# Optimization experiments

Hardware: AMD Instinct MI355X
Metric: run time of the kernel (lower is better)

Reference implementation:

```python
import math
import jax, jax.numpy as jnp
import numpy as np

EPS = 1e-7  # K.epsilon()
ANCHORS = np.array([[10, 14], [23, 27], [37, 58], [81, 82], [135, 169], [344, 319]], np.float32)
ANCHOR_MASK = [[3, 4, 5], [0, 1, 2]]  # tiny-yolo, num_layers = 2
NUM_CLASSES = 80
IGNORE_THRESH = 0.5


def _decode(feats, anchors, input_shape):
    # feats: (B,H,W,3*(5+C)) -> raw_pred (B,H,W,3,5+C), pred_xy, pred_wh (normalized xywh)
    B, H, W, _ = feats.shape
    na = anchors.shape[0]
    feats = feats.reshape(B, H, W, na, 5 + NUM_CLASSES)
    gy, gx = jnp.meshgrid(jnp.arange(H, dtype=feats.dtype), jnp.arange(W, dtype=feats.dtype), indexing='ij')
    grid = jnp.stack([gx, gy], -1)[None, :, :, None, :]  # (1,H,W,1,2) in (x,y)
    box_xy = (jax.nn.sigmoid(feats[..., :2]) + grid) / jnp.array([W, H], feats.dtype)
    box_wh = jnp.exp(feats[..., 2:4]) * anchors[None, None, None, :, :] / input_shape[::-1]
    return feats, box_xy, box_wh


def _box_ciou(b_true, b_pred):
    # b_true: (B,T,4) xywh, b_pred: (B,H,W,A,4) xywh -> ciou, iou: (B,H,W,A,T)
    bt = b_true[:, None, None, None, :, :]   # (B,1,1,1,T,4)
    bp = b_pred[..., None, :]                # (B,H,W,A,1,4)
    t_xy, t_wh = bt[..., :2], bt[..., 2:4]
    p_xy, p_wh = bp[..., :2], bp[..., 2:4]
    t_min, t_max = t_xy - t_wh / 2.0, t_xy + t_wh / 2.0
    p_min, p_max = p_xy - p_wh / 2.0, p_xy + p_wh / 2.0
    i_wh = jnp.maximum(jnp.minimum(t_max, p_max) - jnp.maximum(t_min, p_min), 0.0)
    inter = i_wh[..., 0] * i_wh[..., 1]
    union = t_wh[..., 0] * t_wh[..., 1] + p_wh[..., 0] * p_wh[..., 1] - inter
    iou = inter / (union + EPS)
    center = jnp.sum(jnp.square(t_xy - p_xy), -1)
    e_wh = jnp.maximum(jnp.maximum(t_max, p_max) - jnp.minimum(t_min, p_min), 0.0)
    diag = jnp.sum(jnp.square(e_wh), -1)
    diou = iou - center / (diag + EPS)
    v = 4.0 * jnp.square(jnp.arctan2(t_wh[..., 0], t_wh[..., 1]) - jnp.arctan2(p_wh[..., 0], p_wh[..., 1])) / (math.pi * math.pi)
    alpha = jax.lax.stop_gradient(v / (1.0 - iou + v + EPS))
    return diou - alpha * v, iou


def _bce_logits(target, logits):
    # numerically stable sigmoid BCE with logits (matches K.binary_crossentropy from_logits=True)
    return jnp.maximum(logits, 0.0) - logits * target + jnp.log1p(jnp.exp(-jnp.abs(logits)))


def setup_inputs() -> dict:
    key = jax.random.key(0)
    ks = jax.random.split(key, 10)
    B, T = 64, 100
    output0 = jax.random.normal(ks[0], (B, 13, 13, 255), jnp.float32) * 0.5
    output1 = jax.random.normal(ks[1], (B, 26, 26, 255), jnp.float32) * 0.5
    xy = jax.random.uniform(ks[2], (B, T, 2), jnp.float32)
    wh = jax.random.uniform(ks[3], (B, T, 2), jnp.float32, minval=0.05, maxval=0.3)
    y_true_box = jnp.concatenate([xy, wh], -1)
    iou_mask0 = (jax.random.uniform(ks[4], (B, 13, 13, 3, T)) < 0.01).astype(jnp.float32)
    iou_mask1 = (jax.random.uniform(ks[5], (B, 26, 26, 3, T)) < 0.01).astype(jnp.float32)
    class0 = jax.nn.one_hot(jax.random.randint(ks[6], (B, 13, 13, 3), 0, NUM_CLASSES), NUM_CLASSES) * (jax.random.uniform(ks[7], (B, 13, 13, 3, 1)) < 0.7)
    class1 = jax.nn.one_hot(jax.random.randint(ks[8], (B, 26, 26, 3), 0, NUM_CLASSES), NUM_CLASSES) * (jax.random.uniform(ks[9], (B, 26, 26, 3, 1)) < 0.7)
    return {"output0": output0, "output1": output1, "y_true_box": y_true_box,
            "iou_mask0": iou_mask0, "iou_mask1": iou_mask1, "class0": class0, "class1": class1}


def reference(output0, output1, y_true_box, iou_mask0, iou_mask1, class0, class1):
    outputs = [output0, output1]
    masks = [iou_mask0, iou_mask1]
    classes = [class0, class1]
    input_shape = jnp.asarray(output0.shape[1:3], jnp.float32) * 32.0  # (h,w)
    batch_f = jnp.float32(output0.shape[0])
    loss = total_loc = total_conf = total_cls = jnp.float32(0.0)
    for i in range(2):
        anchors = jnp.asarray(ANCHORS[ANCHOR_MASK[i]])
        raw_pred, pred_xy, pred_wh = _decode(outputs[i], anchors, input_shape)
        pred_box = jnp.concatenate([pred_xy, pred_wh], -1)  # (B,H,W,3,4)
        ciou, iou = _box_ciou(y_true_box, pred_box)         # (B,H,W,3,T)
        best_iou = jnp.max(iou, -1)                         # (B,H,W,3)
        ignore = (best_iou < IGNORE_THRESH)[..., None]
        ignore_match = (best_iou > IGNORE_THRESH)[..., None]
        class_id_match = jax.lax.stop_gradient(
            (jnp.max(jax.nn.sigmoid(raw_pred[..., 5:]), -1) < 0.25)[..., None] & ignore_match)
        ignore_mask = (ignore | class_id_match).astype(jnp.float32)
        ciou_loss = jnp.sum((1.0 - ciou) * masks[i], -1, keepdims=True)  # (B,H,W,3,1)
        obj = jnp.max(masks[i], -1, keepdims=True)  # true_objectness_probs
        bce_obj = _bce_logits(obj, raw_pred[..., 4:5])
        confidence_loss = obj * bce_obj + (1.0 - obj) * bce_obj * ignore_mask
        class_loss = obj * _bce_logits(classes[i], raw_pred[..., 5:])
        class_sum = jnp.sum(classes[i], -1, keepdims=True)
        class_sum = class_sum + (class_sum == 0).astype(jnp.float32)
        location_loss = jnp.sum(ciou_loss / class_sum) / batch_f
        confidence_loss = jnp.sum(confidence_loss) / batch_f
        class_loss = jnp.sum(class_loss) / batch_f
        loss = loss + location_loss + confidence_loss + class_loss
        total_loc = total_loc + location_loss
        total_conf = total_conf + confidence_loss
        total_cls = total_cls + class_loss
    return loss, total_loc, total_conf, total_cls
```

## Files before the change

### kernel.cpp

```cpp
#include <hip/hip_runtime.h>
#include <math.h>

#define T_BOX 100
#define NCLS 80
constexpr float EPSF = 1e-7f;
constexpr float INV416 = 1.0f / 416.0f;
constexpr float LOGIT25 = -1.0986122886681098f;

__device__ __forceinline__ float rcpf_(float x) { return __builtin_amdgcn_rcpf(x); }
__device__ __forceinline__ float sigmoidf_(float x) { return rcpf_(1.0f + __expf(-x)); }
__device__ __forceinline__ float softplus_abs_(float x) {
    return __logf(1.0f + __expf(-fabsf(x)));
}

__device__ __forceinline__ float atan2_pos_(float y, float x) {
    const float mn = fminf(y, x), mx = fmaxf(y, x);
    const float r  = mn * rcpf_(mx);
    const float r2 = r * r;
    float p = fmaf(r2, 0.0208351f, -0.0851330f);
    p = fmaf(r2, p, 0.1801410f);
    p = fmaf(r2, p, -0.3302995f);
    p = fmaf(r2, p, 0.9998660f);
    const float a = r * p;
    return (y > x) ? (1.5707963268f - a) : a;
}

__constant__ float c_anc[2][3][2] = {
    {{81.0f, 82.0f}, {135.0f, 169.0f}, {344.0f, 319.0f}},
    {{10.0f, 14.0f}, {23.0f, 27.0f}, {37.0f, 58.0f}},
};

#define CELLS0 507
#define CELLS1 2028
#define CELLS_TOT 2535
#define GRP_PER_BLK 16
#define NCHUNK 4
#define CELLS_PER_BLK 64
#define BLK_PER_BATCH 40

__device__ __forceinline__ float red16_add(float v) {
    v += __shfl_xor(v, 1); v += __shfl_xor(v, 2);
    v += __shfl_xor(v, 4); v += __shfl_xor(v, 8);
    return v;
}
__device__ __forceinline__ float red16_max(float v) {
    v = fmaxf(v, __shfl_xor(v, 1)); v = fmaxf(v, __shfl_xor(v, 2));
    v = fmaxf(v, __shfl_xor(v, 4)); v = fmaxf(v, __shfl_xor(v, 8));
    return v;
}

__global__ __launch_bounds__(256) void yolo_fused_kernel(
    const float* __restrict__ pred0, const float* __restrict__ mask0, const float* __restrict__ cls0,
    const float* __restrict__ pred1, const float* __restrict__ mask1, const float* __restrict__ cls1,
    const float* __restrict__ ytrue,
    float* __restrict__ ws, int nshard)
{
    __shared__ float4 s_box[T_BOX];
    __shared__ float4 s_aux[T_BOX];
    __shared__ float s_acc[6];

    const int b = blockIdx.y;
    const int tid = threadIdx.x;

    if (tid < T_BOX) {
        const float4 yt = *reinterpret_cast<const float4*>(ytrue + ((size_t)b * T_BOX + tid) * 4);
        s_box[tid] = make_float4(yt.x - 0.5f * yt.z, yt.y - 0.5f * yt.w,
                                 yt.x + 0.5f * yt.z, yt.y + 0.5f * yt.w);
        s_aux[tid] = make_float4(yt.x, yt.y, yt.z * yt.w, atan2_pos_(yt.z, yt.w));
    }
    if (tid < 6) s_acc[tid] = 0.0f;
    __syncthreads();

    const int l   = tid & 15;
    const int grp = tid >> 4;
    const float c4pi2 = 4.0f / (float)(M_PI * M_PI);

    #pragma unroll 1
    for (int chunk = 0; chunk < NCHUNK; ++chunk) {
        const int r = (int)blockIdx.x * CELLS_PER_BLK + chunk * GRP_PER_BLK + grp;
        if (r >= CELLS_TOT) break;

        int level, W, H, cell, ncell;
        const float *pred, *mask, *cls;
        float invWH;
        if (r < CELLS0) {
            level = 0; W = 13; H = 13; cell = r; ncell = CELLS0;
            invWH = 1.0f / 13.0f;
            pred = pred0; mask = mask0; cls = cls0;
        } else {
            level = 1; W = 26; H = 26; cell = r - CELLS0; ncell = CELLS1;
            invWH = 1.0f / 26.0f;
            pred = pred1; mask = mask1; cls = cls1;
        }

        const int a  = cell % 3;
        const int hw = cell / 3;
        const int w  = hw % W;
        const int h  = hw / W;

        const float* p = pred + ((size_t)((b * H + h) * W + w)) * 255 + a * 85;

        const float aw = c_anc[level][a][0];
        const float ah = c_anc[level][a][1];

        const float px = (sigmoidf_(p[0]) + (float)w) * invWH;
        const float py = (sigmoidf_(p[1]) + (float)h) * invWH;
        const float pw = __expf(p[2]) * aw * INV416;
        const float ph = __expf(p[3]) * ah * INV416;

        const float pminx = px - 0.5f * pw, pminy = py - 0.5f * ph;
        const float pmaxx = px + 0.5f * pw, pmaxy = py + 0.5f * ph;
        const float parea = pw * ph;
        const float patan = atan2_pos_(pw, ph);

        const float* m = mask + ((size_t)b * ncell + cell) * (size_t)T_BOX;

        float maxd = -1e30f, obj = 0.0f, locsum = 0.0f;

        float mv_[7];
        #pragma unroll
        for (int k = 0; k < 6; ++k) mv_[k] = m[l + 16 * k];
        mv_[6] = (l < 4) ? m[l + 96] : 0.0f;

        auto body = [&](int t, float mv) {
            const float4 bx = s_box[t];
            const float4 ax = s_aux[t];
            const float iwx = fmaxf(fminf(bx.z, pmaxx) - fmaxf(bx.x, pminx), 0.0f);
            const float iwy = fmaxf(fminf(bx.w, pmaxy) - fmaxf(bx.y, pminy), 0.0f);
            const float inter = iwx * iwy;
            const float sa = ax.z + parea;
            maxd = fmaxf(maxd, fmaf(3.0f, inter, -sa));
            obj  = fmaxf(obj, mv);
            if (mv != 0.0f) {
                const float uni = sa - inter;
                const float iou = inter * rcpf_(uni + EPSF);
                const float dx = ax.x - px, dy = ax.y - py;
                const float center = dx * dx + dy * dy;
                const float ewx = fmaxf(fmaxf(bx.z, pmaxx) - fminf(bx.x, pminx), 0.0f);
                const float ewy = fmaxf(fmaxf(bx.w, pmaxy) - fminf(bx.y, pminy), 0.0f);
                const float diag = ewx * ewx + ewy * ewy;
                const float diou = iou - center * rcpf_(diag + EPSF);
                const float dv = ax.w - patan;
                const float v = c4pi2 * dv * dv;
                const float alpha = v * rcpf_(1.0f - iou + v + EPSF);
                const float ciou = diou - alpha * v;
                locsum += (1.0f - ciou) * mv;
            }
        };

        #pragma unroll
        for (int k = 0; k < 6; ++k) body(l + 16 * k, mv_[k]);
        if (l < 4) body(l + 96, mv_[6]);

        obj  = red16_max(obj);
        maxd = red16_max(maxd);

        const float x4 = p[4];
        const float bce = fmaxf(x4, 0.0f) - x4 * obj + softplus_abs_(x4);

        float loc = 0.0f, conf, clsl = 0.0f;

        if (obj > 0.0f) {
            const float* cp = cls + ((size_t)b * ncell + cell) * (size_t)NCLS;
            float csum = 0.0f, bsum = 0.0f;
            #pragma unroll
            for (int k = 0; k < 5; ++k) {
                const int c = l + 16 * k;
                const float z = cp[c];
                const float x = p[5 + c];
                csum += z;
                bsum += fmaxf(x, 0.0f) - x * z + softplus_abs_(x);
            }
            locsum = red16_add(locsum);
            csum   = red16_add(csum);
            bsum   = red16_add(bsum);
            const float csum2 = csum + ((csum == 0.0f) ? 1.0f : 0.0f);
            loc  = locsum * rcpf_(csum2);
            clsl = bsum;
            conf = bce;
        } else {
            float ign;
            if (maxd > EPSF) {
                float maxlogit = -1e30f;
                #pragma unroll
                for (int k = 0; k < 5; ++k) maxlogit = fmaxf(maxlogit, p[5 + l + 16 * k]);
                maxlogit = red16_max(maxlogit);
                ign = (maxlogit < LOGIT25) ? 1.0f : 0.0f;
            } else {
                ign = (maxd < EPSF) ? 1.0f : 0.0f;
            }
            conf = bce * ign;
        }

        if (l == 0) {
            const int base = level * 3;
            atomicAdd(&s_acc[base + 0], loc);
            atomicAdd(&s_acc[base + 1], conf);
            atomicAdd(&s_acc[base + 2], clsl);
        }
    }

    __syncthreads();
    if (tid < 6) {
        const int shard = (int)((blockIdx.y * gridDim.x + blockIdx.x) % (unsigned)nshard);
        atomicAdd(&ws[shard * 16 + tid], s_acc[tid]);
    }
}

__global__ void yolo_finalize(const float* __restrict__ ws,
                              float* __restrict__ out, float invB, int nshard) {
    __shared__ float s_sum[6];
    const int t = threadIdx.x;
    if (t < 6) {
        float s = 0.0f;
        for (int i = 0; i < nshard; ++i) s += ws[i * 16 + t];
        s_sum[t] = s;
    }
    __syncthreads();
    if (t == 0) {
        const float loc  = (s_sum[0] + s_sum[3]) * invB;
        const float conf = (s_sum[1] + s_sum[4]) * invB;
        const float cls  = (s_sum[2] + s_sum[5]) * invB;
        out[0] = loc + conf + cls;
        out[1] = loc;
        out[2] = conf;
        out[3] = cls;
    }
}

extern "C" void kernel_launch(void* const* d_in, const int* in_sizes, int n_in,
                              void* d_out, int out_size, void* d_ws, size_t ws_size,
                              hipStream_t stream) {
    const float* out0  = (const float*)d_in[0];
    const float* out1  = (const float*)d_in[1];
    const float* ytrue = (const float*)d_in[2];
    const float* m0    = (const float*)d_in[3];
    const float* m1    = (const float*)d_in[4];
    const float* c0    = (const float*)d_in[5];
    const float* c1    = (const float*)d_in[6];
    float* out = (float*)d_out;
    float* ws  = (float*)d_ws;

    const int B = in_sizes[0] / (13 * 13 * 255);

    int nshard = (int)(ws_size / 64);
    if (nshard < 1)  nshard = 1;
    if (nshard > 64) nshard = 64;
    const size_t zero_bytes = (nshard == 1) ? 24 : (size_t)nshard * 64;

    hipMemsetAsync(ws, 0, zero_bytes, stream);

    dim3 grid(BLK_PER_BATCH, B);
    yolo_fused_kernel<<<grid, 256, 0, stream>>>(
        out0, m0, c0, out1, m1, c1, ytrue, ws, nshard);

    yolo_finalize<<<1, 64, 0, stream>>>(ws, out, 1.0f / (float)B, nshard);
}
```

Before: 54.01 us.

## Use 8 lanes per cell, one cell per group, and split aux shared arrays

Each cell is now processed by 8 lanes instead of 16, and the per-block chunk loop is removed, so every group handles one cell and the grid grows to 80 blocks per batch. Each lane walks 12-13 target boxes, which gives more independent mask loads in flight and shortens the shuffle reductions by one step. The mask loads are hoisted ahead of the prediction decode. The float4 aux shared array is split into four scalar arrays so that the common path reads only the area. In exchange, the per-block setup of the shared box tables is repeated across twice as many blocks, and each lane holds more registers.

```diff
diff --git a/kernel.cpp b/kernel.cpp
--- a/kernel.cpp
+++ b/kernel.cpp
@@ -33,19 +33,17 @@
 #define CELLS0 507
 #define CELLS1 2028
 #define CELLS_TOT 2535
-#define GRP_PER_BLK 16
-#define NCHUNK 4
-#define CELLS_PER_BLK 64
-#define BLK_PER_BATCH 40
-
-__device__ __forceinline__ float red16_add(float v) {
-    v += __shfl_xor(v, 1); v += __shfl_xor(v, 2);
-    v += __shfl_xor(v, 4); v += __shfl_xor(v, 8);
+#define LPC 8
+#define GRP_PER_BLK 32
+#define BLK_PER_BATCH 80
+
+__device__ __forceinline__ float red8_add(float v) {
+    v += __shfl_xor(v, 1); v += __shfl_xor(v, 2); v += __shfl_xor(v, 4);
     return v;
 }
-__device__ __forceinline__ float red16_max(float v) {
+__device__ __forceinline__ float red8_max(float v) {
     v = fmaxf(v, __shfl_xor(v, 1)); v = fmaxf(v, __shfl_xor(v, 2));
-    v = fmaxf(v, __shfl_xor(v, 4)); v = fmaxf(v, __shfl_xor(v, 8));
+    v = fmaxf(v, __shfl_xor(v, 4));
     return v;
 }
 
@@ -56,7 +54,7 @@
     float* __restrict__ ws, int nshard)
 {
     __shared__ float4 s_box[T_BOX];
-    __shared__ float4 s_aux[T_BOX];
+    __shared__ float s_ar[T_BOX], s_tx[T_BOX], s_ty[T_BOX], s_at[T_BOX];
     __shared__ float s_acc[6];
 
     const int b = blockIdx.y;
@@ -66,20 +64,18 @@
         const float4 yt = *reinterpret_cast<const float4*>(ytrue + ((size_t)b * T_BOX + tid) * 4);
         s_box[tid] = make_float4(yt.x - 0.5f * yt.z, yt.y - 0.5f * yt.w,
                                  yt.x + 0.5f * yt.z, yt.y + 0.5f * yt.w);
-        s_aux[tid] = make_float4(yt.x, yt.y, yt.z * yt.w, atan2_pos_(yt.z, yt.w));
+        s_ar[tid] = yt.z * yt.w;
+        s_tx[tid] = yt.x; s_ty[tid] = yt.y;
+        s_at[tid] = atan2_pos_(yt.z, yt.w);
     }
     if (tid < 6) s_acc[tid] = 0.0f;
     __syncthreads();
 
-    const int l   = tid & 15;
-    const int grp = tid >> 4;
-    const float c4pi2 = 4.0f / (float)(M_PI * M_PI);
-
-    #pragma unroll 1
-    for (int chunk = 0; chunk < NCHUNK; ++chunk) {
-        const int r = (int)blockIdx.x * CELLS_PER_BLK + chunk * GRP_PER_BLK + grp;
-        if (r >= CELLS_TOT) break;
-
+    const int l   = tid & (LPC - 1);
+    const int grp = tid >> 3;
+    const int r   = (int)blockIdx.x * GRP_PER_BLK + grp;
+
+    if (r < CELLS_TOT) {
         int level, W, H, cell, ncell;
         const float *pred, *mask, *cls;
         float invWH;
@@ -99,6 +95,12 @@
         const int h  = hw / W;
 
         const float* p = pred + ((size_t)((b * H + h) * W + w)) * 255 + a * 85;
+        const float* m = mask + ((size_t)b * ncell + cell) * (size_t)T_BOX;
+
+        float mv_[13];
+        #pragma unroll
+        for (int k = 0; k < 12; ++k) mv_[k] = m[l + LPC * k];
+        mv_[12] = (l < 4) ? m[96 + l] : 0.0f;
 
         const float aw = c_anc[level][a][0];
         const float ah = c_anc[level][a][1];
@@ -112,35 +114,28 @@
         const float pmaxx = px + 0.5f * pw, pmaxy = py + 0.5f * ph;
         const float parea = pw * ph;
         const float patan = atan2_pos_(pw, ph);
-
-        const float* m = mask + ((size_t)b * ncell + cell) * (size_t)T_BOX;
+        const float c4pi2 = 4.0f / (float)(M_PI * M_PI);
 
         float maxd = -1e30f, obj = 0.0f, locsum = 0.0f;
-
-        float mv_[7];
-        #pragma unroll
-        for (int k = 0; k < 6; ++k) mv_[k] = m[l + 16 * k];
-        mv_[6] = (l < 4) ? m[l + 96] : 0.0f;
 
         auto body = [&](int t, float mv) {
             const float4 bx = s_box[t];
-            const float4 ax = s_aux[t];
             const float iwx = fmaxf(fminf(bx.z, pmaxx) - fmaxf(bx.x, pminx), 0.0f);
             const float iwy = fmaxf(fminf(bx.w, pmaxy) - fmaxf(bx.y, pminy), 0.0f);
             const float inter = iwx * iwy;
-            const float sa = ax.z + parea;
+            const float sa = s_ar[t] + parea;
             maxd = fmaxf(maxd, fmaf(3.0f, inter, -sa));
             obj  = fmaxf(obj, mv);
             if (mv != 0.0f) {
                 const float uni = sa - inter;
                 const float iou = inter * rcpf_(uni + EPSF);
-                const float dx = ax.x - px, dy = ax.y - py;
+                const float dx = s_tx[t] - px, dy = s_ty[t] - py;
                 const float center = dx * dx + dy * dy;
                 const float ewx = fmaxf(fmaxf(bx.z, pmaxx) - fminf(bx.x, pminx), 0.0f);
                 const float ewy = fmaxf(fmaxf(bx.w, pmaxy) - fminf(bx.y, pminy), 0.0f);
                 const float diag = ewx * ewx + ewy * ewy;
                 const float diou = iou - center * rcpf_(diag + EPSF);
-                const float dv = ax.w - patan;
+                const float dv = s_at[t] - patan;
                 const float v = c4pi2 * dv * dv;
                 const float alpha = v * rcpf_(1.0f - iou + v + EPSF);
                 const float ciou = diou - alpha * v;
@@ -149,11 +144,11 @@
         };
 
         #pragma unroll
-        for (int k = 0; k < 6; ++k) body(l + 16 * k, mv_[k]);
-        if (l < 4) body(l + 96, mv_[6]);
-
-        obj  = red16_max(obj);
-        maxd = red16_max(maxd);
+        for (int k = 0; k < 12; ++k) body(l + LPC * k, mv_[k]);
+        if (l < 4) body(96 + l, mv_[12]);
+
+        obj  = red8_max(obj);
+        maxd = red8_max(maxd);
 
         const float x4 = p[4];
         const float bce = fmaxf(x4, 0.0f) - x4 * obj + softplus_abs_(x4);
@@ -164,16 +159,16 @@
             const float* cp = cls + ((size_t)b * ncell + cell) * (size_t)NCLS;
             float csum = 0.0f, bsum = 0.0f;
             #pragma unroll
-            for (int k = 0; k < 5; ++k) {
-                const int c = l + 16 * k;
+            for (int k = 0; k < 10; ++k) {
+                const int c = l + LPC * k;
                 const float z = cp[c];
                 const float x = p[5 + c];
                 csum += z;
                 bsum += fmaxf(x, 0.0f) - x * z + softplus_abs_(x);
             }
-            locsum = red16_add(locsum);
-            csum   = red16_add(csum);
-            bsum   = red16_add(bsum);
+            locsum = red8_add(locsum);
+            csum   = red8_add(csum);
+            bsum   = red8_add(bsum);
             const float csum2 = csum + ((csum == 0.0f) ? 1.0f : 0.0f);
             loc  = locsum * rcpf_(csum2);
             clsl = bsum;
@@ -183,8 +178,8 @@
             if (maxd > EPSF) {
                 float maxlogit = -1e30f;
                 #pragma unroll
-                for (int k = 0; k < 5; ++k) maxlogit = fmaxf(maxlogit, p[5 + l + 16 * k]);
-                maxlogit = red16_max(maxlogit);
+                for (int k = 0; k < 10; ++k) maxlogit = fmaxf(maxlogit, p[5 + l + LPC * k]);
+                maxlogit = red8_max(maxlogit);
                 ign = (maxlogit < LOGIT25) ? 1.0f : 0.0f;
             } else {
                 ign = (maxd < EPSF) ? 1.0f : 0.0f;
```

After: 51.64 us. 1.05x faster.
